# Performance work log

Hardware: AMD Instinct MI355X
Metric: run time of the kernel (lower is better)

Reference implementation:

```python
import jax, jax.numpy as jnp
import numpy as np

N_NODES = 50000
EMBED_DIM = 512
N_EDGES = 150000


def _edge_scores(node_embeddings, edges):
    # edges: [2, E] int; dot product of endpoint embeddings -> [E]
    src = node_embeddings[edges[0]]  # [E, D]
    dst = node_embeddings[edges[1]]  # [E, D]
    return jnp.sum(src * dst, axis=1)


def setup_inputs() -> dict:
    key = jax.random.key(0)
    k1, k2, k3 = jax.random.split(key, 3)
    node_embeddings = jax.random.normal(k1, (N_NODES, EMBED_DIM), dtype=jnp.float32)
    edge_index = jax.random.randint(k2, (2, N_EDGES), 0, N_NODES, dtype=jnp.int64)
    # negative edges: uniform random node pairs (matches the original sampler's
    # fallback distribution; precomputed so the reference is deterministic/jittable)
    neg_edges = jax.random.randint(k3, (2, N_EDGES), 0, N_NODES, dtype=jnp.int64)
    return {
        "node_embeddings": node_embeddings,
        "edge_index": edge_index,
        "neg_edges": neg_edges,
        "num_nodes": N_NODES,
    }


def reference(node_embeddings, edge_index, neg_edges, num_nodes):
    pos_scores = _edge_scores(node_embeddings, edge_index)  # [E]
    neg_scores = _edge_scores(node_embeddings, neg_edges)   # [E]
    all_scores = jnp.concatenate([pos_scores, neg_scores])
    all_labels = jnp.concatenate([
        jnp.ones_like(pos_scores),
        jnp.zeros_like(neg_scores),
    ])
    # BCE with logits: log(1 + exp(s)) - s*y, numerically stable via logaddexp
    per_elem = jnp.logaddexp(jnp.float32(0.0), all_scores) - all_scores * all_labels
    return jnp.mean(per_elem)
```

## Files before the change

### kernel.cpp

```cpp
#include <hip/hip_runtime.h>
#include <math.h>

#define N_EDGES   150000
#define TOTAL     300000
#define EMBED_DIM 512
#define N_NODES   50000
#define TABLE_ELEMS (N_NODES * EMBED_DIM)
#define TABLE_BYTES_F8 ((size_t)TABLE_ELEMS)
#define BLOCK_THREADS 256
#define CONV_BLOCKS 2048

#define GROUPS16   (TOTAL / 16)
#define POS_G16    (N_EDGES / 16)

#define NCHUNK       8
#define CHUNK_BYTES  64
#define NODE_UNITS   (N_NODES * 16)
#define CONV_BLOCKS_EXACT (NODE_UNITS / BLOCK_THREADS)
#define SLICE_BYTES  ((size_t)N_NODES * CHUNK_BYTES)
#define PARTIAL_BYTES ((size_t)NCHUNK * TOTAL * 4)
#define WS_ACC_OFF   (TABLE_BYTES_F8 + PARTIAL_BYTES)
#define WS_NEEDED    (WS_ACC_OFF + 64)

#define SCORE_BLOCKS 2048
#define WAVES_PER_CHUNK 1024
#define NB4      ((GROUPS16 + 3) / 4)
#define RED_BLOCKS ((TOTAL + BLOCK_THREADS - 1) / BLOCK_THREADS)

typedef float floatx4 __attribute__((ext_vector_type(4)));
typedef float floatx2 __attribute__((ext_vector_type(2)));
typedef unsigned long long ull;
typedef ull ull2 __attribute__((ext_vector_type(2)));
typedef int  intx2 __attribute__((ext_vector_type(2)));

__global__ __launch_bounds__(BLOCK_THREADS) void convert_fp8_chunked(
    const floatx4* __restrict__ in,
    int*           __restrict__ out,
    float*         __restrict__ acc,
    unsigned int*  __restrict__ cnt)
{
    if (blockIdx.x == 0 && threadIdx.x == 0) { *acc = 0.0f; *cnt = 0u; }
    const int u    = blockIdx.x * BLOCK_THREADS + threadIdx.x;
    const int node = u >> 4;
    const int w4   = u & 15;
    const floatx4* __restrict__ src = in + node * 128 + w4;
    #pragma unroll
    for (int c = 0; c < NCHUNK; c++) {
        floatx4 v = __builtin_nontemporal_load(src + c * 16);
        int r = 0;
        r = __builtin_amdgcn_cvt_pk_fp8_f32(v[0], v[1], r, false);
        r = __builtin_amdgcn_cvt_pk_fp8_f32(v[2], v[3], r, true);
        __builtin_nontemporal_store(r, out + c * NODE_UNITS + u);
    }
}

__device__ __forceinline__ void score8(
    int gb, int i, int quad, int half, int sl8, bool is_diag, int dreg,
    const unsigned char* __restrict__ slice,
    const int* __restrict__ pos_edges, const int* __restrict__ neg_edges,
    float* __restrict__ pout)
{
    int s[8], t[8];
    const bool widepos = (gb + 8 <= POS_G16);
    const bool wideneg = (gb >= POS_G16) && (16 * gb + 128 <= 2 * N_EDGES);
    if (widepos || wideneg) {
        const int* __restrict__ ed = widepos ? pos_edges : neg_edges;
        const int e0 = 16 * gb - (widepos ? 0 : N_EDGES);
        const int lane = threadIdx.x & 63;
        const intx2 sv = __builtin_nontemporal_load((const intx2*)(ed + e0) + lane);
        const intx2 tv = __builtin_nontemporal_load((const intx2*)(ed + N_EDGES + e0) + lane);
        #pragma unroll
        for (int j = 0; j < 8; j++) {
            const int sx = __shfl(sv[0], 8 * j + sl8, 64);
            const int sy = __shfl(sv[1], 8 * j + sl8, 64);
            s[j] = half ? sy : sx;
            const int tx = __shfl(tv[0], 8 * j + sl8, 64);
            const int ty = __shfl(tv[1], 8 * j + sl8, 64);
            t[j] = half ? ty : tx;
        }
    } else {
        #pragma unroll
        for (int j = 0; j < 8; j++) {
            int g = gb + j;
            if (g > GROUPS16 - 1) g = GROUPS16 - 1;
            const bool ip = (g < POS_G16);
            const int* __restrict__ ed = ip ? pos_edges : neg_edges;
            const int e0 = 16 * g - (ip ? 0 : N_EDGES);
            s[j] = __builtin_nontemporal_load(ed + e0 + i);
            t[j] = __builtin_nontemporal_load(ed + N_EDGES + e0 + i);
        }
    }
    ull2 a[8], b[8];
    #pragma unroll
    for (int j = 0; j < 8; j++) {
        a[j] = *(const ull2*)(slice + (size_t)(unsigned)s[j] * CHUNK_BYTES + quad * 16);
        b[j] = *(const ull2*)(slice + (size_t)(unsigned)t[j] * CHUNK_BYTES + quad * 16);
    }
#if __has_builtin(__builtin_amdgcn_sched_barrier)
    __builtin_amdgcn_sched_barrier(0);
#endif
    float scv[8];
    #pragma unroll
    for (int j = 0; j < 8; j++) {
        floatx4 C = {0, 0, 0, 0};
        C = __builtin_amdgcn_mfma_f32_16x16x32_fp8_fp8((long)a[j][0], (long)b[j][0], C, 0, 0, 0);
        C = __builtin_amdgcn_mfma_f32_16x16x32_fp8_fp8((long)a[j][1], (long)b[j][1], C, 0, 0, 0);
        scv[j] = (dreg == 0) ? C[0] : (dreg == 1) ? C[1] : (dreg == 2) ? C[2] : C[3];
    }
    if (gb + 8 <= GROUPS16) {
        const int lane = threadIdx.x & 63;
        const int i0   = (2 * lane) & 15;
        const int src0 = ((i0 >> 2) << 4) + i0;
        const int jsel = lane >> 3;
        float o0 = 0.0f, o1 = 0.0f;
        #pragma unroll
        for (int j = 0; j < 8; j++) {
            const float t0 = __shfl(scv[j], src0, 64);
            const float t1 = __shfl(scv[j], src0 + 1, 64);
            if (jsel == j) { o0 = t0; o1 = t1; }
        }
        floatx2 o = { o0, o1 };
        __builtin_nontemporal_store(o, (floatx2*)(pout + 16 * gb) + lane);
    } else {
        #pragma unroll
        for (int j = 0; j < 8; j++) {
            const int g = gb + j;
            if (is_diag && g < GROUPS16)
                __builtin_nontemporal_store(scv[j], pout + 16 * g + i);
        }
    }
}

__device__ __forceinline__ void score4(
    int gb, int i, int quad, bool is_diag, int dreg,
    const unsigned char* __restrict__ slice,
    const int* __restrict__ pos_edges, const int* __restrict__ neg_edges,
    float* __restrict__ pout)
{
    int s[4], t[4];
    const bool widepos = (gb + 4 <= POS_G16);
    const bool wideneg = (gb >= POS_G16) && (16 * gb + 64 <= 2 * N_EDGES);
    if (widepos || wideneg) {
        const int* __restrict__ ed = widepos ? pos_edges : neg_edges;
        const int e0 = 16 * gb - (widepos ? 0 : N_EDGES);
        const int lane = threadIdx.x & 63;
        const int sv = __builtin_nontemporal_load(ed + e0 + lane);
        const int tv = __builtin_nontemporal_load(ed + N_EDGES + e0 + lane);
        #pragma unroll
        for (int j = 0; j < 4; j++) {
            s[j] = __shfl(sv, 16 * j + i, 64);
            t[j] = __shfl(tv, 16 * j + i, 64);
        }
    } else {
        #pragma unroll
        for (int j = 0; j < 4; j++) {
            int g = gb + j;
            if (g > GROUPS16 - 1) g = GROUPS16 - 1;
            const bool ip = (g < POS_G16);
            const int* __restrict__ ed = ip ? pos_edges : neg_edges;
            const int e0 = 16 * g - (ip ? 0 : N_EDGES);
            s[j] = __builtin_nontemporal_load(ed + e0 + i);
            t[j] = __builtin_nontemporal_load(ed + N_EDGES + e0 + i);
        }
    }
    ull2 a[4], b[4];
    #pragma unroll
    for (int j = 0; j < 4; j++) {
        a[j] = *(const ull2*)(slice + (size_t)(unsigned)s[j] * CHUNK_BYTES + quad * 16);
        b[j] = *(const ull2*)(slice + (size_t)(unsigned)t[j] * CHUNK_BYTES + quad * 16);
    }
#if __has_builtin(__builtin_amdgcn_sched_barrier)
    __builtin_amdgcn_sched_barrier(0);
#endif
    float scv[4];
    #pragma unroll
    for (int j = 0; j < 4; j++) {
        floatx4 C = {0, 0, 0, 0};
        C = __builtin_amdgcn_mfma_f32_16x16x32_fp8_fp8((long)a[j][0], (long)b[j][0], C, 0, 0, 0);
        C = __builtin_amdgcn_mfma_f32_16x16x32_fp8_fp8((long)a[j][1], (long)b[j][1], C, 0, 0, 0);
        scv[j] = (dreg == 0) ? C[0] : (dreg == 1) ? C[1] : (dreg == 2) ? C[2] : C[3];
    }
    if (gb + 4 <= GROUPS16) {
        const int lane = threadIdx.x & 63;
        const int ii   = lane & 15;
        const int src  = ((ii >> 2) << 4) + ii;
        const int jsel = lane >> 4;
        float o = 0.0f;
        #pragma unroll
        for (int j = 0; j < 4; j++) {
            const float tj = __shfl(scv[j], src, 64);
            if (jsel == j) o = tj;
        }
        __builtin_nontemporal_store(o, pout + 16 * gb + lane);
    } else {
        #pragma unroll
        for (int j = 0; j < 4; j++) {
            const int g = gb + j;
            if (is_diag && g < GROUPS16)
                __builtin_nontemporal_store(scv[j], pout + 16 * g + i);
        }
    }
}

__global__ __launch_bounds__(BLOCK_THREADS, 4) void edge_score_chunked(
    const unsigned char* __restrict__ emb8,
    const int*           __restrict__ pos_edges,
    const int*           __restrict__ neg_edges,
    float*               __restrict__ partial)
{
    const int chunk = blockIdx.x & 7;
    const int wid   = (blockIdx.x >> 3) * 4 + (threadIdx.x >> 6);
    const int lane  = threadIdx.x & 63;
    const int i     = lane & 15;
    const int quad  = lane >> 4;
    const bool is_diag = ((i >> 2) == quad);
    const int  dreg = i & 3;
    const int  half = i & 1;
    const int  sl8  = i >> 1;

    const unsigned char* __restrict__ slice = emb8 + (size_t)chunk * SLICE_BYTES;
    float* __restrict__ pout = partial + (size_t)chunk * TOTAL;

    int sp    = (wid * NB4) >> 10;
    const int se = ((wid + 1) * NB4) >> 10;

    for (; sp + 2 <= se; sp += 2)
        score8(4 * sp, i, quad, half, sl8, is_diag, dreg,
               slice, pos_edges, neg_edges, pout);
    if (sp < se)
        score4(4 * sp, i, quad, is_diag, dreg,
               slice, pos_edges, neg_edges, pout);
}

__global__ __launch_bounds__(BLOCK_THREADS) void reduce_bce_finalize(
    const float*  __restrict__ partial,
    float*        __restrict__ acc,
    unsigned int* __restrict__ cnt,
    float*        __restrict__ out)
{
    const int e = blockIdx.x * BLOCK_THREADS + threadIdx.x;
    float term = 0.0f;
    if (e < TOTAL) {
        float s = 0.0f;
        #pragma unroll
        for (int c = 0; c < NCHUNK; c++)
            s += partial[(size_t)c * TOTAL + e];
        const float sp = fmaxf(s, 0.0f) + log1pf(expf(-fabsf(s)));
        term = sp - (e < N_EDGES ? s : 0.0f);
    }
    #pragma unroll
    for (int off = 32; off > 0; off >>= 1)
        term += __shfl_down(term, off, 64);
    __shared__ float ls[4];
    if ((threadIdx.x & 63) == 0) ls[threadIdx.x >> 6] = term;
    __syncthreads();
    if (threadIdx.x == 0) {
        atomicAdd(acc, ls[0] + ls[1] + ls[2] + ls[3]);
        __threadfence();
        const unsigned prev = atomicAdd(cnt, 1u);
        if (prev == (unsigned)(gridDim.x - 1)) {
            __threadfence();
            const float tot = atomicAdd(acc, 0.0f);
            out[0] = tot * (1.0f / (float)TOTAL);
        }
    }
}

__global__ __launch_bounds__(BLOCK_THREADS) void convert_fp8(
    const float4* __restrict__ in,
    int*          __restrict__ out,
    float*        __restrict__ acc)
{
    if (blockIdx.x == 0 && threadIdx.x == 0) *acc = 0.0f;
    const int stride = gridDim.x * blockDim.x;
    for (int i = blockIdx.x * blockDim.x + threadIdx.x;
         i < TABLE_ELEMS / 4; i += stride) {
        float4 v = in[i];
        int r = 0;
        r = __builtin_amdgcn_cvt_pk_fp8_f32(v.x, v.y, r, false);
        r = __builtin_amdgcn_cvt_pk_fp8_f32(v.z, v.w, r, true);
        out[i] = r;
    }
}

#define EDGE_BLOCKS ((GROUPS16 + 3) / 4)
__global__ __launch_bounds__(BLOCK_THREADS, 4) void edge_loss_fp8(
    const unsigned char* __restrict__ emb8,
    const int*           __restrict__ pos_edges,
    const int*           __restrict__ neg_edges,
    float*               __restrict__ acc)
{
    const int wave = threadIdx.x >> 6;
    const int lane = threadIdx.x & 63;
    const int g    = blockIdx.x * 4 + wave;
    const int i    = lane & 15;
    const int quad = lane >> 4;
    const bool is_diag = ((i >> 2) == quad);
    const int  dreg    = i & 3;
    float contrib = 0.0f;
    if (g < GROUPS16) {
        const bool is_pos = (g < POS_G16);
        const int* __restrict__ edges = is_pos ? pos_edges : neg_edges;
        const int  e0 = 16 * g - (is_pos ? 0 : N_EDGES);
        const int sidx = edges[e0 + i];
        const int tidx = edges[N_EDGES + e0 + i];
        const ull2* rA = (const ull2*)(emb8 + (size_t)sidx * EMBED_DIM + quad * 16);
        const ull2* rB = (const ull2*)(emb8 + (size_t)tidx * EMBED_DIM + quad * 16);
        ull2 a[8], b[8];
        #pragma unroll
        for (int c = 0; c < 8; c++) { a[c] = rA[c * 4]; b[c] = rB[c * 4]; }
#if __has_builtin(__builtin_amdgcn_sched_barrier)
        __builtin_amdgcn_sched_barrier(0);
#endif
        floatx4 C0 = {0,0,0,0}, C1 = {0,0,0,0}, C2 = {0,0,0,0}, C3 = {0,0,0,0};
        #pragma unroll
        for (int c = 0; c < 2; c++) {
            #pragma unroll
            for (int h = 0; h < 2; h++) {
                C0 = __builtin_amdgcn_mfma_f32_16x16x32_fp8_fp8((long)a[c][h],     (long)b[c][h],     C0, 0, 0, 0);
                C1 = __builtin_amdgcn_mfma_f32_16x16x32_fp8_fp8((long)a[2 + c][h], (long)b[2 + c][h], C1, 0, 0, 0);
                C2 = __builtin_amdgcn_mfma_f32_16x16x32_fp8_fp8((long)a[4 + c][h], (long)b[4 + c][h], C2, 0, 0, 0);
                C3 = __builtin_amdgcn_mfma_f32_16x16x32_fp8_fp8((long)a[6 + c][h], (long)b[6 + c][h], C3, 0, 0, 0);
            }
        }
        floatx4 C = (C0 + C1) + (C2 + C3);
        float s = (dreg == 0) ? C[0] : (dreg == 1) ? C[1] : (dreg == 2) ? C[2] : C[3];
        float sp = fmaxf(s, 0.0f) + log1pf(expf(-fabsf(s)));
        contrib = is_diag ? (sp - (is_pos ? s : 0.0f)) : 0.0f;
    }
    #pragma unroll
    for (int off = 32; off > 0; off >>= 1)
        contrib += __shfl_down(contrib, off, 64);
    __shared__ float ls[4];
    if (lane == 0) ls[wave] = contrib;
    __syncthreads();
    if (threadIdx.x == 0)
        atomicAdd(acc, ls[0] + ls[1] + ls[2] + ls[3]);
}

#define N_PAIRS   (TOTAL / 2)
#define POS_PAIRS (N_EDGES / 2)
#define FB_WAVES  (CONV_BLOCKS * 4)
__global__ __launch_bounds__(BLOCK_THREADS, 8) void edge_loss_f32(
    const float* __restrict__ emb,
    const int*   __restrict__ pos_edges,
    const int*   __restrict__ neg_edges,
    float*       __restrict__ acc)
{
    const int wave  = threadIdx.x >> 6;
    const int lane  = threadIdx.x & 63;
    const int gwave = blockIdx.x * 4 + wave;
    float lsum = 0.0f;
    for (int g = gwave; g < N_PAIRS; g += FB_WAVES) {
        const bool is_pos = (g < POS_PAIRS);
        const int* __restrict__ edges = is_pos ? pos_edges : neg_edges;
        const int  e0 = 2 * g - (is_pos ? 0 : N_EDGES);
        const int s0 = edges[e0],     t0 = edges[N_EDGES + e0];
        const int s1 = edges[e0 + 1], t1 = edges[N_EDGES + e0 + 1];
        const float4* rS0 = (const float4*)(emb + (size_t)s0 * EMBED_DIM) + lane;
        const float4* rT0 = (const float4*)(emb + (size_t)t0 * EMBED_DIM) + lane;
        const float4* rS1 = (const float4*)(emb + (size_t)s1 * EMBED_DIM) + lane;
        const float4* rT1 = (const float4*)(emb + (size_t)t1 * EMBED_DIM) + lane;
        float4 a0 = rS0[0], a1 = rS0[64];
        float4 b0 = rT0[0], b1 = rT0[64];
        float4 c0 = rS1[0], c1 = rS1[64];
        float4 d0 = rT1[0], d1 = rT1[64];
        float p0 = fmaf(a0.x, b0.x, fmaf(a0.y, b0.y, fmaf(a0.z, b0.z, a0.w * b0.w)));
        float p1 = fmaf(a1.x, b1.x, fmaf(a1.y, b1.y, fmaf(a1.z, b1.z, a1.w * b1.w)));
        float q0 = fmaf(c0.x, d0.x, fmaf(c0.y, d0.y, fmaf(c0.z, d0.z, c0.w * d0.w)));
        float q1 = fmaf(c1.x, d1.x, fmaf(c1.y, d1.y, fmaf(c1.z, d1.z, c1.w * d1.w)));
        float p = p0 + p1, q = q0 + q1;
        #pragma unroll
        for (int off = 32; off > 0; off >>= 1) {
            p += __shfl_down(p, off, 64);
            q += __shfl_down(q, off, 64);
        }
        const float sp_p = fmaxf(p, 0.0f) + log1pf(expf(-fabsf(p)));
        const float sp_q = fmaxf(q, 0.0f) + log1pf(expf(-fabsf(q)));
        lsum += (lane == 0) ? (sp_p + sp_q - (is_pos ? (p + q) : 0.0f)) : 0.0f;
    }
    __shared__ float ls[4];
    if (lane == 0) ls[wave] = lsum;
    __syncthreads();
    if (threadIdx.x == 0)
        atomicAdd(acc, ls[0] + ls[1] + ls[2] + ls[3]);
}

__global__ void finalize_kernel(const float* __restrict__ acc, float* __restrict__ out)
{
    if (threadIdx.x == 0)
        out[0] = acc[0] * (1.0f / (float)TOTAL);
}

extern "C" void kernel_launch(void* const* d_in, const int* in_sizes, int n_in,
                              void* d_out, int out_size, void* d_ws, size_t ws_size,
                              hipStream_t stream) {
    const float* emb = (const float*)d_in[0];
    const int*   pos = (const int*)d_in[1];
    const int*   neg = (const int*)d_in[2];
    float* out = (float*)d_out;

    if (ws_size >= WS_NEEDED) {
        unsigned char* emb8    = (unsigned char*)d_ws;
        float*         partial = (float*)((char*)d_ws + TABLE_BYTES_F8);
        float*         acc     = (float*)((char*)d_ws + WS_ACC_OFF);
        unsigned int*  cnt     = (unsigned int*)((char*)d_ws + WS_ACC_OFF + 4);
        convert_fp8_chunked<<<CONV_BLOCKS_EXACT, BLOCK_THREADS, 0, stream>>>(
            (const floatx4*)emb, (int*)d_ws, acc, cnt);
        edge_score_chunked<<<SCORE_BLOCKS, BLOCK_THREADS, 0, stream>>>(
            emb8, pos, neg, partial);
        reduce_bce_finalize<<<RED_BLOCKS, BLOCK_THREADS, 0, stream>>>(
            partial, acc, cnt, out);
    } else if (ws_size >= TABLE_BYTES_F8 + 64) {
        unsigned char* emb8 = (unsigned char*)d_ws;
        float*         acc  = (float*)((char*)d_ws + TABLE_BYTES_F8);
        convert_fp8<<<CONV_BLOCKS, BLOCK_THREADS, 0, stream>>>(
            (const float4*)emb, (int*)d_ws, acc);
        edge_loss_fp8<<<EDGE_BLOCKS, BLOCK_THREADS, 0, stream>>>(emb8, pos, neg, acc);
        finalize_kernel<<<1, 64, 0, stream>>>(acc, out);
    } else {
        float* acc = (float*)d_ws;
        (void)hipMemsetAsync(acc, 0, sizeof(float), stream);
        edge_loss_f32<<<CONV_BLOCKS, BLOCK_THREADS, 0, stream>>>(emb, pos, neg, acc);
        finalize_kernel<<<1, 64, 0, stream>>>(acc, out);
    }
}
```

Before: 227.1 us.

## Fuse convert, score and reduce into one cooperative kernel with grid syncs

Replaces the three-kernel pipeline (fp8 conversion, chunked MFMA edge scoring, BCE reduction) with one cooperative launch of 1024 persistent blocks that separates the phases with grid.sync(). The aim is to remove two kernel launch gaps and tail drains. The reduction now has each thread handle four edges with vector loads. The fp8 table gathers also switch to nontemporal loads. Risks: grid.sync cost, lower parallelism per phase (1024 blocks instead of 2048 for scoring), and nontemporal hints could hurt cache reuse of the gathered table. If the cooperative launch fails, it falls back to the old three-kernel path.

```diff
diff --git a/kernel.cpp b/kernel.cpp
--- a/kernel.cpp
+++ b/kernel.cpp
@@ -1,5 +1,8 @@
 #include <hip/hip_runtime.h>
+#include <hip/hip_cooperative_groups.h>
 #include <math.h>
+
+namespace cg = cooperative_groups;
 
 #define N_EDGES   150000
 #define TOTAL     300000
@@ -27,20 +30,18 @@
 #define NB4      ((GROUPS16 + 3) / 4)
 #define RED_BLOCKS ((TOTAL + BLOCK_THREADS - 1) / BLOCK_THREADS)
 
+#define FUSED_BLOCKS 1024
+#define FUSED_WPC    512
+
 typedef float floatx4 __attribute__((ext_vector_type(4)));
 typedef float floatx2 __attribute__((ext_vector_type(2)));
 typedef unsigned long long ull;
 typedef ull ull2 __attribute__((ext_vector_type(2)));
 typedef int  intx2 __attribute__((ext_vector_type(2)));
 
-__global__ __launch_bounds__(BLOCK_THREADS) void convert_fp8_chunked(
-    const floatx4* __restrict__ in,
-    int*           __restrict__ out,
-    float*         __restrict__ acc,
-    unsigned int*  __restrict__ cnt)
-{
-    if (blockIdx.x == 0 && threadIdx.x == 0) { *acc = 0.0f; *cnt = 0u; }
-    const int u    = blockIdx.x * BLOCK_THREADS + threadIdx.x;
+__device__ __forceinline__ void convert_unit(
+    const floatx4* __restrict__ in, int* __restrict__ out, int u)
+{
     const int node = u >> 4;
     const int w4   = u & 15;
     const floatx4* __restrict__ src = in + node * 128 + w4;
@@ -93,8 +94,10 @@
     ull2 a[8], b[8];
     #pragma unroll
     for (int j = 0; j < 8; j++) {
-        a[j] = *(const ull2*)(slice + (size_t)(unsigned)s[j] * CHUNK_BYTES + quad * 16);
-        b[j] = *(const ull2*)(slice + (size_t)(unsigned)t[j] * CHUNK_BYTES + quad * 16);
+        a[j] = __builtin_nontemporal_load(
+            (const ull2*)(slice + (size_t)(unsigned)s[j] * CHUNK_BYTES + quad * 16));
+        b[j] = __builtin_nontemporal_load(
+            (const ull2*)(slice + (size_t)(unsigned)t[j] * CHUNK_BYTES + quad * 16));
     }
 #if __has_builtin(__builtin_amdgcn_sched_barrier)
     __builtin_amdgcn_sched_barrier(0);
@@ -166,8 +169,10 @@
     ull2 a[4], b[4];
     #pragma unroll
     for (int j = 0; j < 4; j++) {
-        a[j] = *(const ull2*)(slice + (size_t)(unsigned)s[j] * CHUNK_BYTES + quad * 16);
-        b[j] = *(const ull2*)(slice + (size_t)(unsigned)t[j] * CHUNK_BYTES + quad * 16);
+        a[j] = __builtin_nontemporal_load(
+            (const ull2*)(slice + (size_t)(unsigned)s[j] * CHUNK_BYTES + quad * 16));
+        b[j] = __builtin_nontemporal_load(
+            (const ull2*)(slice + (size_t)(unsigned)t[j] * CHUNK_BYTES + quad * 16));
     }
 #if __has_builtin(__builtin_amdgcn_sched_barrier)
     __builtin_amdgcn_sched_barrier(0);
@@ -200,6 +205,99 @@
                 __builtin_nontemporal_store(scv[j], pout + 16 * g + i);
         }
     }
+}
+
+__global__ __launch_bounds__(BLOCK_THREADS, 4) void fused_all(
+    const floatx4*       __restrict__ in,
+    const int*           __restrict__ pos_edges,
+    const int*           __restrict__ neg_edges,
+    unsigned char*       __restrict__ emb8,
+    float*               __restrict__ partial,
+    float*               __restrict__ acc,
+    unsigned int*        __restrict__ cnt,
+    float*               __restrict__ out)
+{
+    cg::grid_group grid = cg::this_grid();
+    const int tid = blockIdx.x * BLOCK_THREADS + threadIdx.x;
+
+    if (tid == 0) { *acc = 0.0f; *cnt = 0u; }
+    int* __restrict__ emb8i = (int*)emb8;
+    for (int u = tid; u < NODE_UNITS; u += FUSED_BLOCKS * BLOCK_THREADS)
+        convert_unit(in, emb8i, u);
+
+    grid.sync();
+
+    {
+        const int chunk = blockIdx.x & 7;
+        const int wid   = (blockIdx.x >> 3) * 4 + (threadIdx.x >> 6);
+        const int lane  = threadIdx.x & 63;
+        const int i     = lane & 15;
+        const int quad  = lane >> 4;
+        const bool is_diag = ((i >> 2) == quad);
+        const int  dreg = i & 3;
+        const int  half = i & 1;
+        const int  sl8  = i >> 1;
+        const unsigned char* __restrict__ slice = emb8 + (size_t)chunk * SLICE_BYTES;
+        float* __restrict__ pout = partial + (size_t)chunk * TOTAL;
+
+        int sp       = (wid * NB4) >> 9;
+        const int se = ((wid + 1) * NB4) >> 9;
+        for (; sp + 2 <= se; sp += 2)
+            score8(4 * sp, i, quad, half, sl8, is_diag, dreg,
+                   slice, pos_edges, neg_edges, pout);
+        if (sp < se)
+            score4(4 * sp, i, quad, is_diag, dreg,
+                   slice, pos_edges, neg_edges, pout);
+    }
+
+    grid.sync();
+
+    {
+        float tsum = 0.0f;
+        if (tid < TOTAL / 4) {
+            const int e0 = 4 * tid;
+            float s0 = 0.f, s1 = 0.f, s2 = 0.f, s3 = 0.f;
+            #pragma unroll
+            for (int c = 0; c < NCHUNK; c++) {
+                floatx4 v = __builtin_nontemporal_load(
+                    (const floatx4*)(partial + (size_t)c * TOTAL + e0));
+                s0 += v[0]; s1 += v[1]; s2 += v[2]; s3 += v[3];
+            }
+            const bool ip = (e0 < N_EDGES);
+            const float sp0 = fmaxf(s0, 0.f) + log1pf(expf(-fabsf(s0)));
+            const float sp1 = fmaxf(s1, 0.f) + log1pf(expf(-fabsf(s1)));
+            const float sp2 = fmaxf(s2, 0.f) + log1pf(expf(-fabsf(s2)));
+            const float sp3 = fmaxf(s3, 0.f) + log1pf(expf(-fabsf(s3)));
+            tsum = (sp0 + sp1 + sp2 + sp3) - (ip ? (s0 + s1 + s2 + s3) : 0.f);
+        }
+        #pragma unroll
+        for (int off = 32; off > 0; off >>= 1)
+            tsum += __shfl_down(tsum, off, 64);
+        __shared__ float ls[4];
+        if ((threadIdx.x & 63) == 0) ls[threadIdx.x >> 6] = tsum;
+        __syncthreads();
+        if (threadIdx.x == 0) {
+            atomicAdd(acc, ls[0] + ls[1] + ls[2] + ls[3]);
+            __threadfence();
+            const unsigned prev = atomicAdd(cnt, 1u);
+            if (prev == (unsigned)(FUSED_BLOCKS - 1)) {
+                __threadfence();
+                const float tot = atomicAdd(acc, 0.0f);
+                out[0] = tot * (1.0f / (float)TOTAL);
+            }
+        }
+    }
+}
+
+__global__ __launch_bounds__(BLOCK_THREADS) void convert_fp8_chunked(
+    const floatx4* __restrict__ in,
+    int*           __restrict__ out,
+    float*         __restrict__ acc,
+    unsigned int*  __restrict__ cnt)
+{
+    if (blockIdx.x == 0 && threadIdx.x == 0) { *acc = 0.0f; *cnt = 0u; }
+    const int u = blockIdx.x * BLOCK_THREADS + threadIdx.x;
+    convert_unit(in, out, u);
 }
 
 __global__ __launch_bounds__(BLOCK_THREADS, 4) void edge_score_chunked(
@@ -217,13 +315,11 @@
     const int  dreg = i & 3;
     const int  half = i & 1;
     const int  sl8  = i >> 1;
-
     const unsigned char* __restrict__ slice = emb8 + (size_t)chunk * SLICE_BYTES;
     float* __restrict__ pout = partial + (size_t)chunk * TOTAL;
 
-    int sp    = (wid * NB4) >> 10;
+    int sp       = (wid * NB4) >> 10;
     const int se = ((wid + 1) * NB4) >> 10;
-
     for (; sp + 2 <= se; sp += 2)
         score8(4 * sp, i, quad, half, sl8, is_diag, dreg,
                slice, pos_edges, neg_edges, pout);
@@ -405,12 +501,21 @@
         float*         partial = (float*)((char*)d_ws + TABLE_BYTES_F8);
         float*         acc     = (float*)((char*)d_ws + WS_ACC_OFF);
         unsigned int*  cnt     = (unsigned int*)((char*)d_ws + WS_ACC_OFF + 4);
-        convert_fp8_chunked<<<CONV_BLOCKS_EXACT, BLOCK_THREADS, 0, stream>>>(
-            (const floatx4*)emb, (int*)d_ws, acc, cnt);
-        edge_score_chunked<<<SCORE_BLOCKS, BLOCK_THREADS, 0, stream>>>(
-            emb8, pos, neg, partial);
-        reduce_bce_finalize<<<RED_BLOCKS, BLOCK_THREADS, 0, stream>>>(
-            partial, acc, cnt, out);
+
+        const floatx4* in4 = (const floatx4*)emb;
+        void* args[] = { (void*)&in4, (void*)&pos, (void*)&neg, (void*)&emb8,
+                         (void*)&partial, (void*)&acc, (void*)&cnt, (void*)&out };
+        hipError_t err = hipLaunchCooperativeKernel(
+            (const void*)fused_all, dim3(FUSED_BLOCKS), dim3(BLOCK_THREADS),
+            args, 0, stream);
+        if (err != hipSuccess) {
+            convert_fp8_chunked<<<CONV_BLOCKS_EXACT, BLOCK_THREADS, 0, stream>>>(
+                (const floatx4*)emb, (int*)d_ws, acc, cnt);
+            edge_score_chunked<<<SCORE_BLOCKS, BLOCK_THREADS, 0, stream>>>(
+                emb8, pos, neg, partial);
+            reduce_bce_finalize<<<RED_BLOCKS, BLOCK_THREADS, 0, stream>>>(
+                partial, acc, cnt, out);
+        }
     } else if (ws_size >= TABLE_BYTES_F8 + 64) {
         unsigned char* emb8 = (unsigned char*)d_ws;
         float*         acc  = (float*)((char*)d_ws + TABLE_BYTES_F8);
```

New measurement: 523.9 us. 131% more time.
